# Kernel optimization log

Hardware: AMD Instinct MI355X
Metric: run time of the kernel (lower is better)

Reference implementation:

```python
import jax, jax.numpy as jnp
import numpy as np

# hyperparameters (from init_kwargs / repo defaults)
AMP_COEF = 1.0
ARG_COEF = 1.0
SSIM_COEF = 1.0
BETA = 1.0
STFT_COEF = 1e-4
EPS = 1e-8
STFT_F = 12
STFT_S = 4


def _gauss_kernel(size=11, sigma=1.5):
    x = jnp.arange(size, dtype=jnp.float32) - (size - 1) / 2.0
    g = jnp.exp(-0.5 * (x / sigma) ** 2)
    k = jnp.outer(g, g)
    return k / jnp.sum(k)


def _depthwise_filter(img, k):
    # img: [B,H,W,C]; 11x11 gaussian, VALID padding, depthwise (per-channel)
    c = img.shape[-1]
    kern = jnp.tile(k[:, :, None, None], (1, 1, 1, c))  # HWIO, I=1, O=C
    return jax.lax.conv_general_dilated(
        img, kern, (1, 1), 'VALID',
        dimension_numbers=('NHWC', 'HWIO', 'NHWC'),
        feature_group_count=c)


def ssim(x, y, max_val=1.0):
    # faithful to tf.image.ssim defaults: filter 11, sigma 1.5, k1=0.01, k2=0.03
    c1 = (0.01 * max_val) ** 2
    c2 = (0.03 * max_val) ** 2
    k = _gauss_kernel()
    mu_x = _depthwise_filter(x, k)
    mu_y = _depthwise_filter(y, k)
    var_x = _depthwise_filter(x * x, k) - mu_x * mu_x
    var_y = _depthwise_filter(y * y, k) - mu_y * mu_y
    cov = _depthwise_filter(x * y, k) - mu_x * mu_y
    lum = (2.0 * mu_x * mu_y + c1) / (mu_x * mu_x + mu_y * mu_y + c1)
    cs = (2.0 * cov + c2) / (var_x + var_y + c2)
    return jnp.mean(lum * cs, axis=(1, 2, 3))  # [B]


def stft(image, f=STFT_F, s=STFT_S):
    # image: [B,N,N,C] -> batched patchwise 2D FFT, cropped to [:f//2,:f//2]
    n = image.shape[1]
    p = (n - f) // s + 1          # num_conv per axis
    half = f // 2
    rows = (jnp.arange(p) * s)[:, None] + jnp.arange(f)   # [P, f]
    patches = image[:, rows]                              # [B,P,f,N,C]
    patches = patches[:, :, :, rows]                      # [B,P,f,P,f,C]
    patches = jnp.transpose(patches, (0, 1, 3, 2, 4, 5))  # [B,Pi,Pj,f,f,C]
    b, c = image.shape[0], image.shape[-1]
    patches = patches.reshape(b, p * p, f, f, c)          # k = i*P + j ordering
    fft = jnp.fft.fft2(patches.astype(jnp.complex64), axes=(2, 3))
    return fft[:, :, :half, :half, :]                     # [B,P*P,half,half,C]


def _freq_filter(f=STFT_F):
    lin = jnp.linspace(0.0, 1.0, f // 2)[:, None]
    return (lin * lin.T)[:, :, None]                      # [half,half,1]


def setup_inputs() -> dict:
    key = jax.random.key(0)
    k1, k2, k3, k4 = jax.random.split(key, 4)
    B, N, C, L = 32, 160, 3, 128
    return {
        'mean': jax.random.normal(k1, (B, L), dtype=jnp.float32),
        'logvar': jax.random.normal(k2, (B, L), dtype=jnp.float32),
        'x_in': jax.random.uniform(k3, (B, N, N, C), dtype=jnp.float32),
        'x_out': jax.random.uniform(k4, (B, N, N, C), dtype=jnp.float32),
    }


def reference(mean, logvar, x_in, x_out):
    # KLD per sample
    var = jnp.exp(logvar)
    kld = -0.5 * jnp.sum(1.0 + logvar - var - mean * mean, axis=1)  # [B]
    # SSIM recon term
    recons = SSIM_COEF * ssim(x_in, x_out, 1.0)                     # [B]
    # patchwise STFT amp/phase loss ('ours')
    stft_out = stft(x_out, STFT_F, STFT_S)
    stft_in = stft(x_in, STFT_F, STFT_S)
    ff = _freq_filter(STFT_F)                                       # [half,half,1]
    arg_diff = jnp.abs(jnp.angle(stft_out + EPS) - jnp.angle(stft_in + EPS))
    amp_diff = jnp.abs(jnp.abs(stft_out) - jnp.abs(stft_in))
    arg_loss = jnp.sum(arg_diff * ff, axis=(1, 2, 3, 4))            # [B]
    amp_loss = jnp.sum(amp_diff * ff, axis=(1, 2, 3, 4))            # [B]
    stft_loss = ARG_COEF * arg_loss + AMP_COEF * amp_loss
    loss = jnp.mean(BETA * kld + recons + STFT_COEF * stft_loss)
    return loss
```

## Files before the change

### kernel.cpp

```cpp
#include <hip/hip_runtime.h>
#include <hip/hip_fp16.h>
#include <math.h>

#define BATCH 32
#define NPIX 160
#define LDIM 128
#define OUT_SZ 150
#define PLANE 25600

#define THREADS 512
#define N_BLOCKS 3649
#define STFT_RD_OFF 2560
#define SSIM_V_OFF 2880
#define VSTRIDE 1296
#define SMEM_FLOATS 9360

__device__ constexpr float TWC[12] = { 1.f, 0.86602540f, 0.5f, 0.f, -0.5f, -0.86602540f,
                                      -1.f,-0.86602540f,-0.5f, 0.f,  0.5f,  0.86602540f};
__device__ constexpr float TWS[12] = { 0.f,-0.5f,-0.86602540f,-1.f,-0.86602540f,-0.5f,
                                       0.f, 0.5f, 0.86602540f, 1.f, 0.86602540f, 0.5f};

__device__ constexpr float GW[11] = {0.00102838f, 0.00759876f, 0.03600076f, 0.10936070f,
                                     0.21300554f, 0.26601172f, 0.21300554f, 0.10936070f,
                                     0.03600076f, 0.00759876f, 0.00102838f};

__device__ __forceinline__ float fast_atan2f(float y, float x) {
    float ax = fabsf(x), ay = fabsf(y);
    float mx = fmaxf(ax, ay), mn = fminf(ax, ay);
    float z = mn / mx;
    float z2 = z * z;
    float p = fmaf(z2, -0.01172120f, 0.05265332f);
    p = fmaf(z2, p, -0.11643287f);
    p = fmaf(z2, p, 0.19354346f);
    p = fmaf(z2, p, -0.33262347f);
    p = fmaf(z2, p, 0.99997726f);
    p = p * z;
    if (ay > ax) p = 1.57079632679489662f - p;
    if (x < 0.f) p = 3.14159265358979323f - p;
    return (y < 0.f) ? -p : p;
}

__device__ __forceinline__ float4 extract_c(float4 f0, float4 f1, float4 f2, int c) {
    if (c == 0) return make_float4(f0.x, f0.w, f1.z, f2.y);
    if (c == 1) return make_float4(f0.y, f1.x, f1.w, f2.z);
    return make_float4(f0.z, f1.y, f2.x, f2.w);
}

__global__ __launch_bounds__(THREADS) void work_kernel(const float* __restrict__ xin,
                                                       const float* __restrict__ xout,
                                                       const float* __restrict__ mean,
                                                       const float* __restrict__ logvar,
                                                       float* __restrict__ out) {
    __shared__ __align__(16) float SMEM[SMEM_FLOATS];
    __shared__ float sm8[8];
    const int tid = threadIdx.x;
    const int gid = blockIdx.x;
    float acc = 0.f;

    if (gid == 3648) {
        float a = 0.f;
        for (int i = tid; i < BATCH * LDIM; i += THREADS) {
            float m = mean[i], lv = logvar[i];
            a += -0.5f * (1.f + lv - expf(lv) - m * m) * (1.f / 32.f);
        }
        #pragma unroll
        for (int o = 32; o > 0; o >>= 1) a += __shfl_down(a, o, 64);
        if ((tid & 63) == 0) sm8[tid >> 6] = a;
        __syncthreads();
        if (tid == 0) {
            float s = sm8[0];
            #pragma unroll
            for (int i = 1; i < 8; ++i) s += sm8[i];
            atomicAdd(out, s);
        }
        return;
    }

    const int grp = gid / 114, k = gid % 114;

    if (k < 57) {
        int idx = grp * 57 + k;
        int b   = idx / 57;
        int rem = idx % 57;
        int c   = rem / 19;
        int prg = rem % 19;
        int row0 = prg * 8;
        __half2* HXY = (__half2*)SMEM;
        __half2* RD  = (__half2*)(SMEM + STFT_RD_OFF);

        for (int t = tid; t < 640; t += THREADS) {
            int rr = t / 40;
            int cq = t % 40;
            size_t off = ((size_t)(b * 160 + row0 + rr) * 160 + cq * 4) * 3;
            const float4* qa = (const float4*)(xin + off);
            const float4* qb = (const float4*)(xout + off);
            float4 a0 = qa[0], a1 = qa[1], a2 = qa[2];
            float4 b0 = qb[0], b1 = qb[1], b2 = qb[2];
            float4 xa = extract_c(a0, a1, a2, c);
            float4 xb = extract_c(b0, b1, b2, c);
            __half2 h[4] __attribute__((aligned(16)));
            h[0] = __floats2half2_rn(xa.x, xb.x);
            h[1] = __floats2half2_rn(xa.y, xb.y);
            h[2] = __floats2half2_rn(xa.z, xb.z);
            h[3] = __floats2half2_rn(xa.w, xb.w);
            *(float4*)&HXY[rr * 160 + cq * 4] = *(float4*)h;
        }
        __syncthreads();

        for (int t = tid; t < 608; t += THREADS) {
            int pc = t % 38;
            int r  = t / 38;
            float4 raw[3];
            raw[0] = *(const float4*)&HXY[r * 160 + pc * 4];
            raw[1] = *(const float4*)&HXY[r * 160 + pc * 4 + 4];
            raw[2] = *(const float4*)&HXY[r * 160 + pc * 4 + 8];
            const __half2* hp = (const __half2*)raw;
            float xa[12], xb[12];
            #pragma unroll
            for (int j = 0; j < 12; ++j) {
                float2 xy = __half22float2(hp[j]);
                xa[j] = xy.x; xb[j] = xy.y;
            }
            #pragma unroll
            for (int img = 0; img < 2; ++img) {
                const float* x = img ? xb : xa;
                float ev[5] = {x[1]+x[11], x[2]+x[10], x[3]+x[9], x[4]+x[8], x[5]+x[7]};
                float ov[5] = {x[1]-x[11], x[2]-x[10], x[3]-x[9], x[4]-x[8], x[5]-x[7]};
                #pragma unroll
                for (int vv = 0; vv < 5; ++vv) {
                    int v = vv + 1;
                    float re = x[0] + ((v & 1) ? -x[6] : x[6]);
                    float im = 0.f;
                    #pragma unroll
                    for (int j = 1; j <= 5; ++j) {
                        int kk = (v * j) % 12;
                        re = fmaf(ev[j-1], TWC[kk], re);
                        im = fmaf(ov[j-1], TWS[kk], im);
                    }
                    RD[((r * 5 + vv) * 2 + img) * 38 + pc] = __floats2half2_rn(re, im);
                }
            }
        }
        __syncthreads();

        if (tid < 380) {
            int pc = tid % 38;
            int vv = (tid / 38) % 5;
            int g  = tid / 190;
            float FR0[5] = {0,0,0,0,0}, FI0[5] = {0,0,0,0,0};
            float FR1[5] = {0,0,0,0,0}, FI1[5] = {0,0,0,0,0};
            #pragma unroll
            for (int i = 0; i < 6; ++i) {
                int rlo = 4 * g + i, rhi = rlo + 6;
                float2 a0 = __half22float2(RD[((rlo * 5 + vv) * 2 + 0) * 38 + pc]);
                float2 a6 = __half22float2(RD[((rhi * 5 + vv) * 2 + 0) * 38 + pc]);
                float2 b0 = __half22float2(RD[((rlo * 5 + vv) * 2 + 1) * 38 + pc]);
                float2 b6 = __half22float2(RD[((rhi * 5 + vv) * 2 + 1) * 38 + pc]);
                float spR0 = a0.x + a6.x, spI0 = a0.y + a6.y;
                float smR0 = a0.x - a6.x, smI0 = a0.y - a6.y;
                float spR1 = b0.x + b6.x, spI1 = b0.y + b6.y;
                float smR1 = b0.x - b6.x, smI1 = b0.y - b6.y;
                #pragma unroll
                for (int uu = 0; uu < 5; ++uu) {
                    int u = uu + 1;
                    int kk = (u * i) % 12;
                    float cu = TWC[kk], su = TWS[kk];
                    float sR0 = (u & 1) ? smR0 : spR0, sI0 = (u & 1) ? smI0 : spI0;
                    float sR1 = (u & 1) ? smR1 : spR1, sI1 = (u & 1) ? smI1 : spI1;
                    FR0[uu] = fmaf(cu, sR0, fmaf(-su, sI0, FR0[uu]));
                    FI0[uu] = fmaf(cu, sI0, fmaf( su, sR0, FI0[uu]));
                    FR1[uu] = fmaf(cu, sR1, fmaf(-su, sI1, FR1[uu]));
                    FI1[uu] = fmaf(cu, sI1, fmaf( su, sR1, FI1[uu]));
                }
            }
            #pragma unroll
            for (int uu = 0; uu < 5; ++uu) {
                float aI = fast_atan2f(FI0[uu], FR0[uu] + 1e-8f);
                float aO = fast_atan2f(FI1[uu], FR1[uu] + 1e-8f);
                float mI = sqrtf(FR0[uu] * FR0[uu] + FI0[uu] * FI0[uu]);
                float mO = sqrtf(FR1[uu] * FR1[uu] + FI1[uu] * FI1[uu]);
                float ff = (float)((uu + 1) * (vv + 1)) * 0.04f;
                acc += ff * (fabsf(aO - aI) + fabsf(mO - mI));
            }
        }
        acc *= 1e-4f / 32.f;
    } else {
        int idx = grp * 57 + (k - 57);
        int b    = idx / 57;
        int rem  = idx % 57;
        int c    = rem / 19;
        int tile = rem % 19;
        int r0 = tile * 8;
        __half2* HXY = (__half2*)SMEM;

        for (int t = tid; t < 720; t += THREADS) {
            int rr = t / 40;
            int cq = t % 40;
            int row = r0 + rr;
            float4 xa = make_float4(0.f, 0.f, 0.f, 0.f);
            float4 xb = make_float4(0.f, 0.f, 0.f, 0.f);
            if (row < NPIX) {
                size_t off = ((size_t)(b * 160 + row) * 160 + cq * 4) * 3;
                const float4* qa = (const float4*)(xin + off);
                const float4* qb = (const float4*)(xout + off);
                float4 a0 = qa[0], a1 = qa[1], a2 = qa[2];
                float4 b0 = qb[0], b1 = qb[1], b2 = qb[2];
                xa = extract_c(a0, a1, a2, c);
                xb = extract_c(b0, b1, b2, c);
            }
            __half2 h[4] __attribute__((aligned(16)));
            h[0] = __floats2half2_rn(xa.x, xb.x);
            h[1] = __floats2half2_rn(xa.y, xb.y);
            h[2] = __floats2half2_rn(xa.z, xb.z);
            h[3] = __floats2half2_rn(xa.w, xb.w);
            *(float4*)&HXY[rr * 160 + cq * 4] = *(float4*)h;
        }
        __syncthreads();

        for (int t = tid; t < 320; t += THREADS) {
            int orow = t / 40;
            int cbase = (t % 40) * 4;
            float ax[4] = {0,0,0,0}, ay[4] = {0,0,0,0};
            float axx[4] = {0,0,0,0}, ayy[4] = {0,0,0,0}, axy[4] = {0,0,0,0};
            #pragma unroll
            for (int kk = 0; kk < 11; ++kk) {
                float4 raw = *(const float4*)&HXY[(orow + kk) * 160 + cbase];
                const __half2* hp = (const __half2*)&raw;
                float wg = GW[kk];
                #pragma unroll
                for (int o = 0; o < 4; ++o) {
                    float2 xy = __half22float2(hp[o]);
                    ax[o]  += wg * xy.x;          ay[o]  += wg * xy.y;
                    axx[o] += wg * (xy.x * xy.x); ayy[o] += wg * (xy.y * xy.y);
                    axy[o] += wg * (xy.x * xy.y);
                }
            }
            int base = SSIM_V_OFF + orow * 160 + cbase;
            *(float4*)&SMEM[base + 0 * VSTRIDE] = make_float4(ax[0],  ax[1],  ax[2],  ax[3]);
            *(float4*)&SMEM[base + 1 * VSTRIDE] = make_float4(ay[0],  ay[1],  ay[2],  ay[3]);
            *(float4*)&SMEM[base + 2 * VSTRIDE] = make_float4(axx[0], axx[1], axx[2], axx[3]);
            *(float4*)&SMEM[base + 3 * VSTRIDE] = make_float4(ayy[0], ayy[1], ayy[2], ayy[3]);
            *(float4*)&SMEM[base + 4 * VSTRIDE] = make_float4(axy[0], axy[1], axy[2], axy[3]);
        }
        __syncthreads();

        for (int t = tid; t < 600; t += THREADS) {
            int orow = t / 75;
            int oc = (t % 75) * 2;
            float st[5][2];
            #pragma unroll
            for (int p = 0; p < 5; ++p) {
                float vals[12];
                #pragma unroll
                for (int kk = 0; kk < 12; ++kk)
                    vals[kk] = SMEM[SSIM_V_OFF + p * VSTRIDE + orow * 160 + oc + kk];
                float s0 = 0.f, s1 = 0.f;
                #pragma unroll
                for (int kk = 0; kk < 11; ++kk) {
                    s0 += GW[kk] * vals[kk];
                    s1 += GW[kk] * vals[kk + 1];
                }
                st[p][0] = s0; st[p][1] = s1;
            }
            const float c1 = 1e-4f, c2 = 9e-4f;
            if (r0 + orow < OUT_SZ) {
                #pragma unroll
                for (int o = 0; o < 2; ++o) {
                    float mx = st[0][o], my = st[1][o];
                    float vx = st[2][o] - mx * mx;
                    float vy = st[3][o] - my * my;
                    float cv = st[4][o] - mx * my;
                    float lum = (2.f * mx * my + c1) / (mx * mx + my * my + c1);
                    float cs  = (2.f * cv + c2) / (vx + vy + c2);
                    acc += lum * cs;
                }
            }
        }
        acc *= 1.f / (32.f * 150.f * 150.f * 3.f);
    }

    #pragma unroll
    for (int o = 32; o > 0; o >>= 1) acc += __shfl_down(acc, o, 64);
    if ((tid & 63) == 0) sm8[tid >> 6] = acc;
    __syncthreads();
    if (tid == 0) {
        float s = sm8[0];
        #pragma unroll
        for (int i = 1; i < 8; ++i) s += sm8[i];
        atomicAdd(out, s);
    }
}

extern "C" void kernel_launch(void* const* d_in, const int* in_sizes, int n_in,
                              void* d_out, int out_size, void* d_ws, size_t ws_size,
                              hipStream_t stream) {
    const float* mean   = (const float*)d_in[0];
    const float* logvar = (const float*)d_in[1];
    const float* xin    = (const float*)d_in[2];
    const float* xout   = (const float*)d_in[3];
    float* out = (float*)d_out;

    hipMemsetAsync(out, 0, sizeof(float), stream);
    work_kernel<<<N_BLOCKS, THREADS, 0, stream>>>(xin, xout, mean, logvar, out);
}
```

Before: 128.5 us.

## Fuse STFT and SSIM tile work into one block sharing the staged input tile

Each block now handles both the STFT patch work and the SSIM work for the same (batch, channel, row-tile), instead of separate blocks for each. The packed half2 input tile is loaded from global memory once and reused by both stages, which halves global input traffic and the block count. The cost is longer per-block serial work with extra barriers, fewer blocks for latency hiding, and STFT rows staged with zero padding past the image edge.

```diff
diff --git a/kernel.cpp b/kernel.cpp
--- a/kernel.cpp
+++ b/kernel.cpp
@@ -6,12 +6,10 @@
 #define NPIX 160
 #define LDIM 128
 #define OUT_SZ 150
-#define PLANE 25600
 
 #define THREADS 512
-#define N_BLOCKS 3649
-#define STFT_RD_OFF 2560
-#define SSIM_V_OFF 2880
+#define N_BLOCKS 1825
+#define SCRATCH_OFF 2880
 #define VSTRIDE 1296
 #define SMEM_FLOATS 9360
 
@@ -57,7 +55,7 @@
     const int gid = blockIdx.x;
     float acc = 0.f;
 
-    if (gid == 3648) {
+    if (gid == 1824) {
         float a = 0.f;
         for (int i = tid; i < BATCH * LDIM; i += THREADS) {
             float m = mean[i], lv = logvar[i];
@@ -76,174 +74,147 @@
         return;
     }
 
-    const int grp = gid / 114, k = gid % 114;
-
-    if (k < 57) {
-        int idx = grp * 57 + k;
-        int b   = idx / 57;
-        int rem = idx % 57;
-        int c   = rem / 19;
-        int prg = rem % 19;
-        int row0 = prg * 8;
-        __half2* HXY = (__half2*)SMEM;
-        __half2* RD  = (__half2*)(SMEM + STFT_RD_OFF);
-
-        for (int t = tid; t < 640; t += THREADS) {
-            int rr = t / 40;
-            int cq = t % 40;
-            size_t off = ((size_t)(b * 160 + row0 + rr) * 160 + cq * 4) * 3;
+    int b    = gid / 57;
+    int rem  = gid % 57;
+    int c    = rem / 19;
+    int tile = rem % 19;
+    int r0 = tile * 8;
+    __half2* HXY = (__half2*)SMEM;
+    __half2* RD  = (__half2*)(SMEM + SCRATCH_OFF);
+
+    for (int t = tid; t < 720; t += THREADS) {
+        int rr = t / 40;
+        int cq = t % 40;
+        int row = r0 + rr;
+        float4 xa = make_float4(0.f, 0.f, 0.f, 0.f);
+        float4 xb = make_float4(0.f, 0.f, 0.f, 0.f);
+        if (row < NPIX) {
+            size_t off = ((size_t)(b * 160 + row) * 160 + cq * 4) * 3;
             const float4* qa = (const float4*)(xin + off);
             const float4* qb = (const float4*)(xout + off);
             float4 a0 = qa[0], a1 = qa[1], a2 = qa[2];
             float4 b0 = qb[0], b1 = qb[1], b2 = qb[2];
-            float4 xa = extract_c(a0, a1, a2, c);
-            float4 xb = extract_c(b0, b1, b2, c);
-            __half2 h[4] __attribute__((aligned(16)));
-            h[0] = __floats2half2_rn(xa.x, xb.x);
-            h[1] = __floats2half2_rn(xa.y, xb.y);
-            h[2] = __floats2half2_rn(xa.z, xb.z);
-            h[3] = __floats2half2_rn(xa.w, xb.w);
-            *(float4*)&HXY[rr * 160 + cq * 4] = *(float4*)h;
-        }
-        __syncthreads();
-
-        for (int t = tid; t < 608; t += THREADS) {
-            int pc = t % 38;
-            int r  = t / 38;
-            float4 raw[3];
-            raw[0] = *(const float4*)&HXY[r * 160 + pc * 4];
-            raw[1] = *(const float4*)&HXY[r * 160 + pc * 4 + 4];
-            raw[2] = *(const float4*)&HXY[r * 160 + pc * 4 + 8];
-            const __half2* hp = (const __half2*)raw;
-            float xa[12], xb[12];
-            #pragma unroll
-            for (int j = 0; j < 12; ++j) {
-                float2 xy = __half22float2(hp[j]);
-                xa[j] = xy.x; xb[j] = xy.y;
-            }
-            #pragma unroll
-            for (int img = 0; img < 2; ++img) {
-                const float* x = img ? xb : xa;
-                float ev[5] = {x[1]+x[11], x[2]+x[10], x[3]+x[9], x[4]+x[8], x[5]+x[7]};
-                float ov[5] = {x[1]-x[11], x[2]-x[10], x[3]-x[9], x[4]-x[8], x[5]-x[7]};
-                #pragma unroll
-                for (int vv = 0; vv < 5; ++vv) {
-                    int v = vv + 1;
-                    float re = x[0] + ((v & 1) ? -x[6] : x[6]);
-                    float im = 0.f;
-                    #pragma unroll
-                    for (int j = 1; j <= 5; ++j) {
-                        int kk = (v * j) % 12;
-                        re = fmaf(ev[j-1], TWC[kk], re);
-                        im = fmaf(ov[j-1], TWS[kk], im);
-                    }
-                    RD[((r * 5 + vv) * 2 + img) * 38 + pc] = __floats2half2_rn(re, im);
+            xa = extract_c(a0, a1, a2, c);
+            xb = extract_c(b0, b1, b2, c);
+        }
+        __half2 h[4] __attribute__((aligned(16)));
+        h[0] = __floats2half2_rn(xa.x, xb.x);
+        h[1] = __floats2half2_rn(xa.y, xb.y);
+        h[2] = __floats2half2_rn(xa.z, xb.z);
+        h[3] = __floats2half2_rn(xa.w, xb.w);
+        *(float4*)&HXY[rr * 160 + cq * 4] = *(float4*)h;
+    }
+    __syncthreads();
+
+    for (int t = tid; t < 608; t += THREADS) {
+        int pc = t % 38;
+        int r  = t / 38;
+        float4 raw[3];
+        raw[0] = *(const float4*)&HXY[r * 160 + pc * 4];
+        raw[1] = *(const float4*)&HXY[r * 160 + pc * 4 + 4];
+        raw[2] = *(const float4*)&HXY[r * 160 + pc * 4 + 8];
+        const __half2* hp = (const __half2*)raw;
+        float xa[12], xb[12];
+        #pragma unroll
+        for (int j = 0; j < 12; ++j) {
+            float2 xy = __half22float2(hp[j]);
+            xa[j] = xy.x; xb[j] = xy.y;
+        }
+        #pragma unroll
+        for (int img = 0; img < 2; ++img) {
+            const float* x = img ? xb : xa;
+            float ev[5] = {x[1]+x[11], x[2]+x[10], x[3]+x[9], x[4]+x[8], x[5]+x[7]};
+            float ov[5] = {x[1]-x[11], x[2]-x[10], x[3]-x[9], x[4]-x[8], x[5]-x[7]};
+            #pragma unroll
+            for (int vv = 0; vv < 5; ++vv) {
+                int v = vv + 1;
+                float re = x[0] + ((v & 1) ? -x[6] : x[6]);
+                float im = 0.f;
+                #pragma unroll
+                for (int j = 1; j <= 5; ++j) {
+                    int kk = (v * j) % 12;
+                    re = fmaf(ev[j-1], TWC[kk], re);
+                    im = fmaf(ov[j-1], TWS[kk], im);
                 }
-            }
-        }
-        __syncthreads();
-
-        if (tid < 380) {
-            int pc = tid % 38;
-            int vv = (tid / 38) % 5;
-            int g  = tid / 190;
-            float FR0[5] = {0,0,0,0,0}, FI0[5] = {0,0,0,0,0};
-            float FR1[5] = {0,0,0,0,0}, FI1[5] = {0,0,0,0,0};
-            #pragma unroll
-            for (int i = 0; i < 6; ++i) {
-                int rlo = 4 * g + i, rhi = rlo + 6;
-                float2 a0 = __half22float2(RD[((rlo * 5 + vv) * 2 + 0) * 38 + pc]);
-                float2 a6 = __half22float2(RD[((rhi * 5 + vv) * 2 + 0) * 38 + pc]);
-                float2 b0 = __half22float2(RD[((rlo * 5 + vv) * 2 + 1) * 38 + pc]);
-                float2 b6 = __half22float2(RD[((rhi * 5 + vv) * 2 + 1) * 38 + pc]);
-                float spR0 = a0.x + a6.x, spI0 = a0.y + a6.y;
-                float smR0 = a0.x - a6.x, smI0 = a0.y - a6.y;
-                float spR1 = b0.x + b6.x, spI1 = b0.y + b6.y;
-                float smR1 = b0.x - b6.x, smI1 = b0.y - b6.y;
-                #pragma unroll
-                for (int uu = 0; uu < 5; ++uu) {
-                    int u = uu + 1;
-                    int kk = (u * i) % 12;
-                    float cu = TWC[kk], su = TWS[kk];
-                    float sR0 = (u & 1) ? smR0 : spR0, sI0 = (u & 1) ? smI0 : spI0;
-                    float sR1 = (u & 1) ? smR1 : spR1, sI1 = (u & 1) ? smI1 : spI1;
-                    FR0[uu] = fmaf(cu, sR0, fmaf(-su, sI0, FR0[uu]));
-                    FI0[uu] = fmaf(cu, sI0, fmaf( su, sR0, FI0[uu]));
-                    FR1[uu] = fmaf(cu, sR1, fmaf(-su, sI1, FR1[uu]));
-                    FI1[uu] = fmaf(cu, sI1, fmaf( su, sR1, FI1[uu]));
-                }
-            }
+                RD[((r * 5 + vv) * 2 + img) * 38 + pc] = __floats2half2_rn(re, im);
+            }
+        }
+    }
+    __syncthreads();
+
+    if (tid < 380) {
+        int pc = tid % 38;
+        int vv = (tid / 38) % 5;
+        int g  = tid / 190;
+        float FR0[5] = {0,0,0,0,0}, FI0[5] = {0,0,0,0,0};
+        float FR1[5] = {0,0,0,0,0}, FI1[5] = {0,0,0,0,0};
+        #pragma unroll
+        for (int i = 0; i < 6; ++i) {
+            int rlo = 4 * g + i, rhi = rlo + 6;
+            float2 a0 = __half22float2(RD[((rlo * 5 + vv) * 2 + 0) * 38 + pc]);
+            float2 a6 = __half22float2(RD[((rhi * 5 + vv) * 2 + 0) * 38 + pc]);
+            float2 b0 = __half22float2(RD[((rlo * 5 + vv) * 2 + 1) * 38 + pc]);
+            float2 b6 = __half22float2(RD[((rhi * 5 + vv) * 2 + 1) * 38 + pc]);
+            float spR0 = a0.x + a6.x, spI0 = a0.y + a6.y;
+            float smR0 = a0.x - a6.x, smI0 = a0.y - a6.y;
+            float spR1 = b0.x + b6.x, spI1 = b0.y + b6.y;
+            float smR1 = b0.x - b6.x, smI1 = b0.y - b6.y;
             #pragma unroll
             for (int uu = 0; uu < 5; ++uu) {
-                float aI = fast_atan2f(FI0[uu], FR0[uu] + 1e-8f);
-                float aO = fast_atan2f(FI1[uu], FR1[uu] + 1e-8f);
-                float mI = sqrtf(FR0[uu] * FR0[uu] + FI0[uu] * FI0[uu]);
-                float mO = sqrtf(FR1[uu] * FR1[uu] + FI1[uu] * FI1[uu]);
-                float ff = (float)((uu + 1) * (vv + 1)) * 0.04f;
-                acc += ff * (fabsf(aO - aI) + fabsf(mO - mI));
-            }
-        }
-        acc *= 1e-4f / 32.f;
-    } else {
-        int idx = grp * 57 + (k - 57);
-        int b    = idx / 57;
-        int rem  = idx % 57;
-        int c    = rem / 19;
-        int tile = rem % 19;
-        int r0 = tile * 8;
-        __half2* HXY = (__half2*)SMEM;
-
-        for (int t = tid; t < 720; t += THREADS) {
-            int rr = t / 40;
-            int cq = t % 40;
-            int row = r0 + rr;
-            float4 xa = make_float4(0.f, 0.f, 0.f, 0.f);
-            float4 xb = make_float4(0.f, 0.f, 0.f, 0.f);
-            if (row < NPIX) {
-                size_t off = ((size_t)(b * 160 + row) * 160 + cq * 4) * 3;
-                const float4* qa = (const float4*)(xin + off);
-                const float4* qb = (const float4*)(xout + off);
-                float4 a0 = qa[0], a1 = qa[1], a2 = qa[2];
-                float4 b0 = qb[0], b1 = qb[1], b2 = qb[2];
-                xa = extract_c(a0, a1, a2, c);
-                xb = extract_c(b0, b1, b2, c);
-            }
-            __half2 h[4] __attribute__((aligned(16)));
-            h[0] = __floats2half2_rn(xa.x, xb.x);
-            h[1] = __floats2half2_rn(xa.y, xb.y);
-            h[2] = __floats2half2_rn(xa.z, xb.z);
-            h[3] = __floats2half2_rn(xa.w, xb.w);
-            *(float4*)&HXY[rr * 160 + cq * 4] = *(float4*)h;
-        }
-        __syncthreads();
-
-        for (int t = tid; t < 320; t += THREADS) {
-            int orow = t / 40;
-            int cbase = (t % 40) * 4;
-            float ax[4] = {0,0,0,0}, ay[4] = {0,0,0,0};
-            float axx[4] = {0,0,0,0}, ayy[4] = {0,0,0,0}, axy[4] = {0,0,0,0};
-            #pragma unroll
-            for (int kk = 0; kk < 11; ++kk) {
-                float4 raw = *(const float4*)&HXY[(orow + kk) * 160 + cbase];
-                const __half2* hp = (const __half2*)&raw;
-                float wg = GW[kk];
-                #pragma unroll
-                for (int o = 0; o < 4; ++o) {
-                    float2 xy = __half22float2(hp[o]);
-                    ax[o]  += wg * xy.x;          ay[o]  += wg * xy.y;
-                    axx[o] += wg * (xy.x * xy.x); ayy[o] += wg * (xy.y * xy.y);
-                    axy[o] += wg * (xy.x * xy.y);
-                }
-            }
-            int base = SSIM_V_OFF + orow * 160 + cbase;
-            *(float4*)&SMEM[base + 0 * VSTRIDE] = make_float4(ax[0],  ax[1],  ax[2],  ax[3]);
-            *(float4*)&SMEM[base + 1 * VSTRIDE] = make_float4(ay[0],  ay[1],  ay[2],  ay[3]);
-            *(float4*)&SMEM[base + 2 * VSTRIDE] = make_float4(axx[0], axx[1], axx[2], axx[3]);
-            *(float4*)&SMEM[base + 3 * VSTRIDE] = make_float4(ayy[0], ayy[1], ayy[2], ayy[3]);
-            *(float4*)&SMEM[base + 4 * VSTRIDE] = make_float4(axy[0], axy[1], axy[2], axy[3]);
-        }
-        __syncthreads();
-
+                int u = uu + 1;
+                int kk = (u * i) % 12;
+                float cu = TWC[kk], su = TWS[kk];
+                float sR0 = (u & 1) ? smR0 : spR0, sI0 = (u & 1) ? smI0 : spI0;
+                float sR1 = (u & 1) ? smR1 : spR1, sI1 = (u & 1) ? smI1 : spI1;
+                FR0[uu] = fmaf(cu, sR0, fmaf(-su, sI0, FR0[uu]));
+                FI0[uu] = fmaf(cu, sI0, fmaf( su, sR0, FI0[uu]));
+                FR1[uu] = fmaf(cu, sR1, fmaf(-su, sI1, FR1[uu]));
+                FI1[uu] = fmaf(cu, sI1, fmaf( su, sR1, FI1[uu]));
+            }
+        }
+        float sacc = 0.f;
+        #pragma unroll
+        for (int uu = 0; uu < 5; ++uu) {
+            float aI = fast_atan2f(FI0[uu], FR0[uu] + 1e-8f);
+            float aO = fast_atan2f(FI1[uu], FR1[uu] + 1e-8f);
+            float mI = sqrtf(FR0[uu] * FR0[uu] + FI0[uu] * FI0[uu]);
+            float mO = sqrtf(FR1[uu] * FR1[uu] + FI1[uu] * FI1[uu]);
+            float ff = (float)((uu + 1) * (vv + 1)) * 0.04f;
+            sacc += ff * (fabsf(aO - aI) + fabsf(mO - mI));
+        }
+        acc += sacc * (1e-4f / 32.f);
+    }
+    __syncthreads();
+
+    for (int t = tid; t < 320; t += THREADS) {
+        int orow = t / 40;
+        int cbase = (t % 40) * 4;
+        float ax[4] = {0,0,0,0}, ay[4] = {0,0,0,0};
+        float axx[4] = {0,0,0,0}, ayy[4] = {0,0,0,0}, axy[4] = {0,0,0,0};
+        #pragma unroll
+        for (int kk = 0; kk < 11; ++kk) {
+            float4 raw = *(const float4*)&HXY[(orow + kk) * 160 + cbase];
+            const __half2* hp = (const __half2*)&raw;
+            float wg = GW[kk];
+            #pragma unroll
+            for (int o = 0; o < 4; ++o) {
+                float2 xy = __half22float2(hp[o]);
+                ax[o]  += wg * xy.x;          ay[o]  += wg * xy.y;
+                axx[o] += wg * (xy.x * xy.x); ayy[o] += wg * (xy.y * xy.y);
+                axy[o] += wg * (xy.x * xy.y);
+            }
+        }
+        int base = SCRATCH_OFF + orow * 160 + cbase;
+        *(float4*)&SMEM[base + 0 * VSTRIDE] = make_float4(ax[0],  ax[1],  ax[2],  ax[3]);
+        *(float4*)&SMEM[base + 1 * VSTRIDE] = make_float4(ay[0],  ay[1],  ay[2],  ay[3]);
+        *(float4*)&SMEM[base + 2 * VSTRIDE] = make_float4(axx[0], axx[1], axx[2], axx[3]);
+        *(float4*)&SMEM[base + 3 * VSTRIDE] = make_float4(ayy[0], ayy[1], ayy[2], ayy[3]);
+        *(float4*)&SMEM[base + 4 * VSTRIDE] = make_float4(axy[0], axy[1], axy[2], axy[3]);
+    }
+    __syncthreads();
+
+    {
+        float hacc = 0.f;
         for (int t = tid; t < 600; t += THREADS) {
             int orow = t / 75;
             int oc = (t % 75) * 2;
@@ -253,7 +224,7 @@
                 float vals[12];
                 #pragma unroll
                 for (int kk = 0; kk < 12; ++kk)
-                    vals[kk] = SMEM[SSIM_V_OFF + p * VSTRIDE + orow * 160 + oc + kk];
+                    vals[kk] = SMEM[SCRATCH_OFF + p * VSTRIDE + orow * 160 + oc + kk];
                 float s0 = 0.f, s1 = 0.f;
                 #pragma unroll
                 for (int kk = 0; kk < 11; ++kk) {
@@ -272,11 +243,11 @@
                     float cv = st[4][o] - mx * my;
                     float lum = (2.f * mx * my + c1) / (mx * mx + my * my + c1);
                     float cs  = (2.f * cv + c2) / (vx + vy + c2);
-                    acc += lum * cs;
+                    hacc += lum * cs;
                 }
             }
         }
-        acc *= 1.f / (32.f * 150.f * 150.f * 3.f);
+        acc += hacc * (1.f / (32.f * 150.f * 150.f * 3.f));
     }
 
     #pragma unroll
```

Result: faster. 123.8 us (-3.6%).
